# Kernel optimization log

Measured on AMD Instinct MI355X. Metric: run time of the kernel, lower is better.

The kernel has to match this reference:

```python
import jax, jax.numpy as jnp
import numpy as np

B, N, M = 2, 2048, 2048
D = 1024          # query_dim == context_dim == inner_dim
H, DH = 16, 64    # heads, dim_head
SCALE = DH ** -0.5


def setup_inputs() -> dict:
    key = jax.random.key(0)
    ks = jax.random.split(key, 7)
    s = 0.02
    return {
        "x": jax.random.normal(ks[0], (B, N, D), jnp.float32),
        "context": jax.random.normal(ks[1], (B, M, D), jnp.float32),
        "Wq": jax.random.normal(ks[2], (D, H * DH), jnp.float32) * s,
        "Wk": jax.random.normal(ks[3], (D, H * DH), jnp.float32) * s,
        "Wv": jax.random.normal(ks[4], (D, H * DH), jnp.float32) * s,
        "Wo": jax.random.normal(ks[5], (H * DH, D), jnp.float32) * s,
        "bo": jax.random.normal(ks[6], (D,), jnp.float32) * s,
    }


def reference(x, context, Wq, Wk, Wv, Wo, bo):
    # Linear projections (bias-free, as in to_q/to_k/to_v)
    q = (x @ Wq).reshape(B, N, H, DH)        # [B,N,H,DH]
    k = (context @ Wk).reshape(B, M, H, DH)  # [B,M,H,DH]
    v = (context @ Wv).reshape(B, M, H, DH)
    # QK^T * scale, softmax over keys, then AV
    sim = jnp.einsum('bnhd,bmhd->bhnm', q, k) * SCALE  # [B,H,N,M]
    attn = jax.nn.softmax(sim, axis=-1)
    out = jnp.einsum('bhnm,bmhd->bnhd', attn, v)       # [B,N,H,DH]
    out = out.reshape(B, N, H * DH)
    return out @ Wo + bo  # to_out Linear; dropout=0 is identity
```

## Files before the change

### kernel.cpp

```cpp
#include <hip/hip_runtime.h>

#define B_  2
#define N_  2048
#define M_  2048
#define D_  1024
#define H_  16
#define DH_ 64

typedef __bf16 bf16x8 __attribute__((ext_vector_type(8)));
typedef __bf16 bf16x4 __attribute__((ext_vector_type(4)));
typedef short  short4v __attribute__((ext_vector_type(4)));
typedef float  f32x4  __attribute__((ext_vector_type(4)));
typedef unsigned int u32x4v __attribute__((ext_vector_type(4)));

#define GAS(p) ((__attribute__((address_space(1))) void*)(p))
#define LAS(p) ((__attribute__((address_space(3))) void*)(p))

#define QPRESCALE 0.18033688011112042f

__device__ __forceinline__ unsigned short f2bf(float f) {
    unsigned int u = __builtin_bit_cast(unsigned int, f);
    u += 0x7fffu + ((u >> 16) & 1u);
    return (unsigned short)(u >> 16);
}

__device__ __forceinline__ unsigned cvtpkbf(float a, float b) {
    unsigned r;
    asm("v_cvt_pk_bf16_f32 %0, %1, %2" : "=v"(r) : "v"(a), "v"(b));
    return r;
}

__global__ __launch_bounds__(256) void prep(
    const float* __restrict__ x, const float* __restrict__ ctx,
    const float* __restrict__ Wq, const float* __restrict__ Wk,
    const float* __restrict__ Wv, const float* __restrict__ Wo,
    unsigned short* __restrict__ xb, unsigned short* __restrict__ cb,
    unsigned short* __restrict__ WTbase)
{
    if (blockIdx.z == 4) {
        int blk = blockIdx.y * 32 + blockIdx.x;
        int stride = 1024 * 256;
        for (int i = blk * 256 + threadIdx.x; i < 2097152; i += stride) {
            const float4* src; unsigned short* dst; int j;
            if (i < 1048576) { src = (const float4*)x;   dst = xb; j = i; }
            else             { src = (const float4*)ctx; dst = cb; j = i - 1048576; }
            float4 v = src[j];
            ushort4 o = make_ushort4(f2bf(v.x), f2bf(v.y), f2bf(v.z), f2bf(v.w));
            *(ushort4*)(dst + 4*j) = o;
        }
        return;
    }
    const float* W = (blockIdx.z == 0) ? Wq : (blockIdx.z == 1) ? Wk
                    : (blockIdx.z == 2) ? Wv : Wo;
    unsigned short* WT = WTbase + (size_t)blockIdx.z * 1048576;
    __shared__ unsigned short t[32][33];
    int tx = threadIdx.x & 31, ty8 = threadIdx.x >> 5;
    int c = blockIdx.x * 32 + tx;
#pragma unroll
    for (int i = 0; i < 4; ++i) {
        int r = blockIdx.y * 32 + i*8 + ty8;
        t[i*8 + ty8][tx] = f2bf(W[(size_t)r * 1024 + c]);
    }
    __syncthreads();
    int c2 = blockIdx.y * 32 + tx;
#pragma unroll
    for (int i = 0; i < 4; ++i) {
        int r2 = blockIdx.x * 32 + i*8 + ty8;
        WT[(size_t)r2 * 1024 + c2] = t[tx][i*8 + ty8];
    }
}

__global__ __launch_bounds__(256) void gemm128(
    const unsigned short* __restrict__ xb,
    const unsigned short* __restrict__ cb,
    const unsigned short* __restrict__ wT,
    const unsigned short* __restrict__ aoA,
    unsigned short* __restrict__ qkv_out,
    const float* __restrict__ bo,
    float* __restrict__ outF,
    int base_mode)
{
    __shared__ __align__(16) unsigned short As[2][128*32];
    __shared__ __align__(16) unsigned short Bs[2][128*32];

    const int mode = base_mode + blockIdx.z;
    const unsigned short* Amat;
    const unsigned short* Bt;
    if (mode == 0)      { Amat = wT;               Bt = xb; }
    else if (mode == 1) { Amat = wT + 1048576;     Bt = cb; }
    else if (mode == 2) { Amat = cb;               Bt = wT + 2*1048576; }
    else                { Amat = wT + 3*1048576;   Bt = aoA; }

    const int tid = threadIdx.x;
    const int w = tid >> 6, l = tid & 63;
    const int quad = l >> 4, l16 = l & 15;
    const int wm = w & 1, wn = w >> 1;
    int row0, col0;
    if (mode == 2) { row0 = blockIdx.x * 128; col0 = blockIdx.y * 128; }
    else           { row0 = blockIdx.y * 128; col0 = blockIdx.x * 128; }

    f32x4 acc[4][4];
#pragma unroll
    for (int i = 0; i < 4; ++i)
#pragma unroll
        for (int j = 0; j < 4; ++j) acc[i][j] = (f32x4){0.f, 0.f, 0.f, 0.f};

    for (int k0 = 0; k0 < 1024; k0 += 64) {
        __syncthreads();
#pragma unroll
        for (int h = 0; h < 2; ++h) {
#pragma unroll
            for (int i = 0; i < 2; ++i) {
                int s = i*256 + w*64 + l;
                int m = s >> 2, c = s & 3;
                int cs = c ^ ((m >> 1) & 3);
                __builtin_amdgcn_global_load_lds(
                    GAS(Amat + (size_t)(row0 + m)*1024 + k0 + h*32 + cs*8),
                    LAS(As[h] + (i*256 + w*64)*8), 16, 0, 0);
                __builtin_amdgcn_global_load_lds(
                    GAS(Bt + (size_t)(col0 + m)*1024 + k0 + h*32 + cs*8),
                    LAS(Bs[h] + (i*256 + w*64)*8), 16, 0, 0);
            }
        }
        __syncthreads();

#pragma unroll
        for (int h = 0; h < 2; ++h) {
            bf16x8 af[4], bfr[4];
#pragma unroll
            for (int mt = 0; mt < 4; ++mt) {
                int m = wm*64 + mt*16 + l16;
                af[mt] = *reinterpret_cast<const bf16x8*>(As[h] + m*32 + (quad ^ ((m >> 1) & 3))*8);
                int n = wn*64 + mt*16 + l16;
                bfr[mt] = *reinterpret_cast<const bf16x8*>(Bs[h] + n*32 + (quad ^ ((n >> 1) & 3))*8);
            }
#pragma unroll
            for (int mt = 0; mt < 4; ++mt)
#pragma unroll
                for (int nt = 0; nt < 4; ++nt)
                    acc[mt][nt] = __builtin_amdgcn_mfma_f32_16x16x32_bf16(
                        af[mt], bfr[nt], acc[mt][nt], 0, 0, 0);
        }
    }

    if (mode == 2) {
#pragma unroll
        for (int mt = 0; mt < 4; ++mt) {
            int gr = row0 + wm*64 + mt*16 + quad*4;
            int b = gr >> 11, nidx = gr & 2047;
#pragma unroll
            for (int nt = 0; nt < 4; ++nt) {
                int col = col0 + wn*64 + nt*16 + l16;
                int h = col >> 6, d = col & 63;
                ushort4 pk = make_ushort4(f2bf(acc[mt][nt][0]), f2bf(acc[mt][nt][1]),
                                          f2bf(acc[mt][nt][2]), f2bf(acc[mt][nt][3]));
                *(ushort4*)(qkv_out + (size_t)2*4194304
                            + (size_t)((b*16 + h)*64 + d)*2048 + nidx) = pk;
            }
        }
    } else {
        const float qs = (mode == 0) ? QPRESCALE : 1.0f;
        unsigned short* obase = qkv_out + (size_t)mode*4194304;
#pragma unroll
        for (int nt = 0; nt < 4; ++nt) {
            int n = col0 + wn*64 + nt*16 + l16;
            int b = n >> 11, nidx = n & 2047;
#pragma unroll
            for (int mt = 0; mt < 4; ++mt) {
                int c = row0 + wm*64 + mt*16 + quad*4;
                int h = c >> 6, d = c & 63;
                ushort4 pkv = make_ushort4(
                    f2bf(acc[mt][nt][0] * qs), f2bf(acc[mt][nt][1] * qs),
                    f2bf(acc[mt][nt][2] * qs), f2bf(acc[mt][nt][3] * qs));
                *(ushort4*)(obase + (size_t)((b*16 + h)*2048 + nidx)*64 + d) = pkv;
            }
        }
    }
}

__global__ __launch_bounds__(256) void gemm_out(
    const unsigned short* __restrict__ woT,
    const unsigned short* __restrict__ aoA,
    const float* __restrict__ bo,
    float* __restrict__ outF)
{
    __shared__ __align__(16) unsigned short As[64*32];
    __shared__ __align__(16) unsigned short Bs[128*32];

    const int tid = threadIdx.x;
    const int w = tid >> 6, l = tid & 63;
    const int quad = l >> 4, l16 = l & 15;
    const int row0 = blockIdx.y * 64;
    const int col0 = blockIdx.x * 128;

    f32x4 acc[4][2];
#pragma unroll
    for (int i = 0; i < 4; ++i)
#pragma unroll
        for (int j = 0; j < 2; ++j) acc[i][j] = (f32x4){0.f, 0.f, 0.f, 0.f};

    for (int k0 = 0; k0 < 1024; k0 += 32) {
        __syncthreads();
        {
            int m = tid >> 2, c = tid & 3;
            int cs = c ^ ((m >> 1) & 3);
            __builtin_amdgcn_global_load_lds(
                GAS(woT + (size_t)(row0 + m)*1024 + k0 + cs*8),
                LAS(As + (w*64)*8), 16, 0, 0);
        }
#pragma unroll
        for (int i = 0; i < 2; ++i) {
            int s = i*256 + tid;
            int m = s >> 2, c = s & 3;
            int cs = c ^ ((m >> 1) & 3);
            __builtin_amdgcn_global_load_lds(
                GAS(aoA + (size_t)(col0 + m)*1024 + k0 + cs*8),
                LAS(Bs + (i*256 + w*64)*8), 16, 0, 0);
        }
        __syncthreads();

        bf16x8 af[4], bfr[2];
#pragma unroll
        for (int mt = 0; mt < 4; ++mt) {
            int m = mt*16 + l16;
            af[mt] = *reinterpret_cast<const bf16x8*>(As + m*32 + (quad ^ ((m >> 1) & 3))*8);
        }
#pragma unroll
        for (int nt = 0; nt < 2; ++nt) {
            int n = w*32 + nt*16 + l16;
            bfr[nt] = *reinterpret_cast<const bf16x8*>(Bs + n*32 + (quad ^ ((n >> 1) & 3))*8);
        }
#pragma unroll
        for (int mt = 0; mt < 4; ++mt)
#pragma unroll
            for (int nt = 0; nt < 2; ++nt)
                acc[mt][nt] = __builtin_amdgcn_mfma_f32_16x16x32_bf16(
                    af[mt], bfr[nt], acc[mt][nt], 0, 0, 0);
    }

#pragma unroll
    for (int mt = 0; mt < 4; ++mt) {
        int c = row0 + mt*16 + quad*4;
        float4 bv = *(const float4*)(bo + c);
#pragma unroll
        for (int nt = 0; nt < 2; ++nt) {
            int n = col0 + w*32 + nt*16 + l16;
            float4 ov = make_float4(acc[mt][nt][0] + bv.x, acc[mt][nt][1] + bv.y,
                                    acc[mt][nt][2] + bv.z, acc[mt][nt][3] + bv.w);
            *(float4*)(outF + (size_t)n*1024 + c) = ov;
        }
    }
}

__global__ __launch_bounds__(256, 2) void flash_attn(
    const unsigned short* __restrict__ qw,
    const unsigned short* __restrict__ kw,
    const unsigned short* __restrict__ vtw,
    unsigned short* __restrict__ ao)
{
    __shared__ __align__(16) unsigned short Tile[2][9216];

    const int tid = threadIdx.x;
    const int w = tid >> 6, l = tid & 63;
    const int quad = l >> 4, l16 = l & 15;
    const int bh = blockIdx.z * H_ + blockIdx.y;
    const int q0 = blockIdx.x * 128 + w * 32;

    int goff[5];
#pragma unroll
    for (int i = 0; i < 5; ++i) {
        int n = i*256 + w*64 + l;
        int m = (n < 576) ? n : n - 576;
        int row = m / 9, c = m % 9;  if (c > 7) c = 7;
        goff[i] = (n < 576) ? row*64 + c*8 : row*2048 + c*8;
    }
    const unsigned short* kbase = kw + (size_t)bh*131072;
    const unsigned short* vbase = vtw + (size_t)bh*131072;

    bf16x8 qf[2][2];
#pragma unroll
    for (int qg = 0; qg < 2; ++qg)
#pragma unroll
        for (int s = 0; s < 2; ++s)
            qf[qg][s] = *reinterpret_cast<const bf16x8*>(
                qw + (size_t)(bh*2048 + q0 + qg*16 + l16)*64 + s*32 + quad*8);

    f32x4 accO[2][4];
#pragma unroll
    for (int qg = 0; qg < 2; ++qg)
#pragma unroll
        for (int td = 0; td < 4; ++td) accO[qg][td] = (f32x4){0.f, 0.f, 0.f, 0.f};
    float lpart[2] = {0.f, 0.f};

    const f32x4 zz = (f32x4){0.f, 0.f, 0.f, 0.f};

    {
#pragma unroll
        for (int i = 0; i < 4; ++i) {
            const unsigned short* bp = (i*4 + w < 9) ? kbase : vbase;
            __builtin_amdgcn_global_load_lds(GAS(bp + goff[i]),
                LAS(&Tile[0][(i*256 + w*64)*8]), 16, 0, 0);
        }
        if (w < 2)
            __builtin_amdgcn_global_load_lds(GAS(vbase + goff[4]),
                LAS(&Tile[0][(1024 + w*64)*8]), 16, 0, 0);
    }

    for (int it = 0; it < 32; ++it) {
        __syncthreads();
        const int cur = it & 1;

        if (it + 1 < 32) {
            const unsigned short* kp = kbase + (it+1)*4096;
            const unsigned short* vp = vbase + (it+1)*64;
#pragma unroll
            for (int i = 0; i < 4; ++i) {
                const unsigned short* bp = (i*4 + w < 9) ? kp : vp;
                __builtin_amdgcn_global_load_lds(GAS(bp + goff[i]),
                    LAS(&Tile[cur^1][(i*256 + w*64)*8]), 16, 0, 0);
            }
            if (w < 2)
                __builtin_amdgcn_global_load_lds(GAS(vp + goff[4]),
                    LAS(&Tile[cur^1][(1024 + w*64)*8]), 16, 0, 0);
        }

        const unsigned short* Ks = &Tile[cur][0];
        const unsigned short* Vs = &Tile[cur][4608];

        f32x4 sac[2][4];
        __builtin_amdgcn_s_setprio(1);
#pragma unroll
        for (int t = 0; t < 4; ++t) {
            const unsigned short* krow = Ks + (t*16 + l16)*72 + quad*8;
            bf16x8 kf0 = *reinterpret_cast<const bf16x8*>(krow);
            bf16x8 kf1 = *reinterpret_cast<const bf16x8*>(krow + 32);
            sac[0][t] = __builtin_amdgcn_mfma_f32_16x16x32_bf16(kf0, qf[0][0], zz, 0, 0, 0);
            sac[1][t] = __builtin_amdgcn_mfma_f32_16x16x32_bf16(kf0, qf[1][0], zz, 0, 0, 0);
            sac[0][t] = __builtin_amdgcn_mfma_f32_16x16x32_bf16(kf1, qf[0][1], sac[0][t], 0, 0, 0);
            sac[1][t] = __builtin_amdgcn_mfma_f32_16x16x32_bf16(kf1, qf[1][1], sac[1][t], 0, 0, 0);
        }
        __builtin_amdgcn_s_setprio(0);

        u32x4v pB[2][2];
#pragma unroll
        for (int qg = 0; qg < 2; ++qg) {
            float s0 = 0.f, s1 = 0.f, s2 = 0.f, s3 = 0.f;
#pragma unroll
            for (int t2 = 0; t2 < 2; ++t2) {
                float pe0 = __builtin_amdgcn_exp2f(sac[qg][2*t2][0]);
                float pe1 = __builtin_amdgcn_exp2f(sac[qg][2*t2][1]);
                float pe2 = __builtin_amdgcn_exp2f(sac[qg][2*t2][2]);
                float pe3 = __builtin_amdgcn_exp2f(sac[qg][2*t2][3]);
                float po0 = __builtin_amdgcn_exp2f(sac[qg][2*t2+1][0]);
                float po1 = __builtin_amdgcn_exp2f(sac[qg][2*t2+1][1]);
                float po2 = __builtin_amdgcn_exp2f(sac[qg][2*t2+1][2]);
                float po3 = __builtin_amdgcn_exp2f(sac[qg][2*t2+1][3]);
                s0 += pe0 + po0; s1 += pe1 + po1;
                s2 += pe2 + po2; s3 += pe3 + po3;
                unsigned b0 = cvtpkbf(pe0, pe1), b1 = cvtpkbf(pe2, pe3);
                unsigned b2 = cvtpkbf(po0, po1), b3 = cvtpkbf(po2, po3);
                asm("v_permlane32_swap_b32 %0, %1" : "+v"(b0), "+v"(b2));
                asm("v_permlane16_swap_b32 %0, %1" : "+v"(b0), "+v"(b2));
                asm("v_permlane32_swap_b32 %0, %1" : "+v"(b1), "+v"(b3));
                asm("v_permlane16_swap_b32 %0, %1" : "+v"(b1), "+v"(b3));
                pB[qg][t2] = (u32x4v){b0, b1, b2, b3};
            }
            lpart[qg] += (s0 + s1) + (s2 + s3);
        }

        __builtin_amdgcn_s_setprio(1);
#pragma unroll
        for (int td = 0; td < 4; ++td) {
            const unsigned short* vrow = Vs + (td*16 + l16)*72 + quad*8;
#pragma unroll
            for (int t2 = 0; t2 < 2; ++t2) {
                bf16x8 vf = *reinterpret_cast<const bf16x8*>(vrow + t2*32);
                accO[0][td] = __builtin_amdgcn_mfma_f32_16x16x32_bf16(
                    vf, __builtin_bit_cast(bf16x8, pB[0][t2]), accO[0][td], 0, 0, 0);
                accO[1][td] = __builtin_amdgcn_mfma_f32_16x16x32_bf16(
                    vf, __builtin_bit_cast(bf16x8, pB[1][t2]), accO[1][td], 0, 0, 0);
            }
        }
        __builtin_amdgcn_s_setprio(0);
    }

#pragma unroll
    for (int qg = 0; qg < 2; ++qg) {
        float s = lpart[qg];
        s += __shfl_xor(s, 16);
        s += __shfl_xor(s, 32);
        float inv = 1.f / s;
        const size_t rowbase =
            (size_t)(blockIdx.z*2048 + q0 + qg*16 + l16)*1024 + blockIdx.y*64;
#pragma unroll
        for (int td = 0; td < 4; ++td)
#pragma unroll
            for (int r = 0; r < 4; ++r)
                ao[rowbase + td*16 + quad*4 + r] = f2bf(accO[qg][td][r] * inv);
    }
}

extern "C" void kernel_launch(void* const* d_in, const int* in_sizes, int n_in,
                              void* d_out, int out_size, void* d_ws, size_t ws_size,
                              hipStream_t stream)
{
    const float* x   = (const float*)d_in[0];
    const float* ctx = (const float*)d_in[1];
    const float* Wq  = (const float*)d_in[2];
    const float* Wk  = (const float*)d_in[3];
    const float* Wv  = (const float*)d_in[4];
    const float* Wo  = (const float*)d_in[5];
    const float* bo  = (const float*)d_in[6];
    float* out = (float*)d_out;

    unsigned short* ws  = (unsigned short*)d_ws;
    unsigned short* xb  = ws;
    unsigned short* cb  = ws + 4194304;
    unsigned short* wT  = ws + 8388608;
    unsigned short* qkv = ws + 12582912;
    unsigned short* ao  = ws;

    prep<<<dim3(32, 32, 5), dim3(256), 0, stream>>>(x, ctx, Wq, Wk, Wv, Wo, xb, cb, wT);
    gemm128<<<dim3(32, 8, 3), dim3(256), 0, stream>>>(xb, cb, wT, ao, qkv, bo, out, 0);
    flash_attn<<<dim3(16, 16, 2), dim3(256), 0, stream>>>(qkv, qkv + 4194304, qkv + 8388608, ao);
    gemm_out<<<dim3(32, 16), dim3(256), 0, stream>>>(wT + 3*1048576, ao, bo, out);
}
```

Measured before the change: 201.0 us.

## Split KV tile across warp pairs in flash attention; double K-step in out-proj GEMM

Flash attention now gives each warp 64 queries and half of each 64-key tile, instead of 32 queries over all keys. This halves the K/V LDS fragment reads per query and lets each loaded K/V fragment feed four MFMAs. The two halves' partial outputs and row sums are reduced through LDS at the end. The output-projection GEMM now loads two 32-wide K slices per barrier pair, halving the number of syncs. The cost is more registers per warp in attention, an extra LDS reduction step, and only half the warps doing the final store.

```diff
diff --git a/kernel.cpp b/kernel.cpp
--- a/kernel.cpp
+++ b/kernel.cpp
@@ -184,8 +184,8 @@
     const float* __restrict__ bo,
     float* __restrict__ outF)
 {
-    __shared__ __align__(16) unsigned short As[64*32];
-    __shared__ __align__(16) unsigned short Bs[128*32];
+    __shared__ __align__(16) unsigned short As[2][64*32];
+    __shared__ __align__(16) unsigned short Bs[2][128*32];
 
     const int tid = threadIdx.x;
     const int w = tid >> 6, l = tid & 63;
@@ -199,43 +199,49 @@
 #pragma unroll
         for (int j = 0; j < 2; ++j) acc[i][j] = (f32x4){0.f, 0.f, 0.f, 0.f};
 
-    for (int k0 = 0; k0 < 1024; k0 += 32) {
+    for (int k0 = 0; k0 < 1024; k0 += 64) {
         __syncthreads();
-        {
-            int m = tid >> 2, c = tid & 3;
-            int cs = c ^ ((m >> 1) & 3);
-            __builtin_amdgcn_global_load_lds(
-                GAS(woT + (size_t)(row0 + m)*1024 + k0 + cs*8),
-                LAS(As + (w*64)*8), 16, 0, 0);
-        }
-#pragma unroll
-        for (int i = 0; i < 2; ++i) {
-            int s = i*256 + tid;
-            int m = s >> 2, c = s & 3;
-            int cs = c ^ ((m >> 1) & 3);
-            __builtin_amdgcn_global_load_lds(
-                GAS(aoA + (size_t)(col0 + m)*1024 + k0 + cs*8),
-                LAS(Bs + (i*256 + w*64)*8), 16, 0, 0);
+#pragma unroll
+        for (int h = 0; h < 2; ++h) {
+            {
+                int m = tid >> 2, c = tid & 3;
+                int cs = c ^ ((m >> 1) & 3);
+                __builtin_amdgcn_global_load_lds(
+                    GAS(woT + (size_t)(row0 + m)*1024 + k0 + h*32 + cs*8),
+                    LAS(As[h] + (w*64)*8), 16, 0, 0);
+            }
+#pragma unroll
+            for (int i = 0; i < 2; ++i) {
+                int s = i*256 + tid;
+                int m = s >> 2, c = s & 3;
+                int cs = c ^ ((m >> 1) & 3);
+                __builtin_amdgcn_global_load_lds(
+                    GAS(aoA + (size_t)(col0 + m)*1024 + k0 + h*32 + cs*8),
+                    LAS(Bs[h] + (i*256 + w*64)*8), 16, 0, 0);
+            }
         }
         __syncthreads();
 
-        bf16x8 af[4], bfr[2];
-#pragma unroll
-        for (int mt = 0; mt < 4; ++mt) {
-            int m = mt*16 + l16;
-            af[mt] = *reinterpret_cast<const bf16x8*>(As + m*32 + (quad ^ ((m >> 1) & 3))*8);
-        }
-#pragma unroll
-        for (int nt = 0; nt < 2; ++nt) {
-            int n = w*32 + nt*16 + l16;
-            bfr[nt] = *reinterpret_cast<const bf16x8*>(Bs + n*32 + (quad ^ ((n >> 1) & 3))*8);
-        }
-#pragma unroll
-        for (int mt = 0; mt < 4; ++mt)
-#pragma unroll
-            for (int nt = 0; nt < 2; ++nt)
-                acc[mt][nt] = __builtin_amdgcn_mfma_f32_16x16x32_bf16(
-                    af[mt], bfr[nt], acc[mt][nt], 0, 0, 0);
+#pragma unroll
+        for (int h = 0; h < 2; ++h) {
+            bf16x8 af[4], bfr[2];
+#pragma unroll
+            for (int mt = 0; mt < 4; ++mt) {
+                int m = mt*16 + l16;
+                af[mt] = *reinterpret_cast<const bf16x8*>(As[h] + m*32 + (quad ^ ((m >> 1) & 3))*8);
+            }
+#pragma unroll
+            for (int nt = 0; nt < 2; ++nt) {
+                int n = w*32 + nt*16 + l16;
+                bfr[nt] = *reinterpret_cast<const bf16x8*>(Bs[h] + n*32 + (quad ^ ((n >> 1) & 3))*8);
+            }
+#pragma unroll
+            for (int mt = 0; mt < 4; ++mt)
+#pragma unroll
+                for (int nt = 0; nt < 2; ++nt)
+                    acc[mt][nt] = __builtin_amdgcn_mfma_f32_16x16x32_bf16(
+                        af[mt], bfr[nt], acc[mt][nt], 0, 0, 0);
+        }
     }
 
 #pragma unroll
@@ -264,7 +270,8 @@
     const int w = tid >> 6, l = tid & 63;
     const int quad = l >> 4, l16 = l & 15;
     const int bh = blockIdx.z * H_ + blockIdx.y;
-    const int q0 = blockIdx.x * 128 + w * 32;
+    const int qh = w & 1, kvh = w >> 1;
+    const int q0 = blockIdx.x * 128 + qh * 64;
 
     int goff[5];
 #pragma unroll
@@ -277,20 +284,20 @@
     const unsigned short* kbase = kw + (size_t)bh*131072;
     const unsigned short* vbase = vtw + (size_t)bh*131072;
 
-    bf16x8 qf[2][2];
-#pragma unroll
-    for (int qg = 0; qg < 2; ++qg)
+    bf16x8 qf[4][2];
+#pragma unroll
+    for (int qg = 0; qg < 4; ++qg)
 #pragma unroll
         for (int s = 0; s < 2; ++s)
             qf[qg][s] = *reinterpret_cast<const bf16x8*>(
                 qw + (size_t)(bh*2048 + q0 + qg*16 + l16)*64 + s*32 + quad*8);
 
-    f32x4 accO[2][4];
-#pragma unroll
-    for (int qg = 0; qg < 2; ++qg)
+    f32x4 accO[4][4];
+#pragma unroll
+    for (int qg = 0; qg < 4; ++qg)
 #pragma unroll
         for (int td = 0; td < 4; ++td) accO[qg][td] = (f32x4){0.f, 0.f, 0.f, 0.f};
-    float lpart[2] = {0.f, 0.f};
+    float lpart[4] = {0.f, 0.f, 0.f, 0.f};
 
     const f32x4 zz = (f32x4){0.f, 0.f, 0.f, 0.f};
 
@@ -327,76 +334,92 @@
         const unsigned short* Ks = &Tile[cur][0];
         const unsigned short* Vs = &Tile[cur][4608];
 
-        f32x4 sac[2][4];
+        f32x4 sac[4][2];
         __builtin_amdgcn_s_setprio(1);
 #pragma unroll
-        for (int t = 0; t < 4; ++t) {
-            const unsigned short* krow = Ks + (t*16 + l16)*72 + quad*8;
+        for (int t = 0; t < 2; ++t) {
+            const unsigned short* krow = Ks + (kvh*32 + t*16 + l16)*72 + quad*8;
             bf16x8 kf0 = *reinterpret_cast<const bf16x8*>(krow);
             bf16x8 kf1 = *reinterpret_cast<const bf16x8*>(krow + 32);
-            sac[0][t] = __builtin_amdgcn_mfma_f32_16x16x32_bf16(kf0, qf[0][0], zz, 0, 0, 0);
-            sac[1][t] = __builtin_amdgcn_mfma_f32_16x16x32_bf16(kf0, qf[1][0], zz, 0, 0, 0);
-            sac[0][t] = __builtin_amdgcn_mfma_f32_16x16x32_bf16(kf1, qf[0][1], sac[0][t], 0, 0, 0);
-            sac[1][t] = __builtin_amdgcn_mfma_f32_16x16x32_bf16(kf1, qf[1][1], sac[1][t], 0, 0, 0);
+#pragma unroll
+            for (int qg = 0; qg < 4; ++qg) {
+                sac[qg][t] = __builtin_amdgcn_mfma_f32_16x16x32_bf16(kf0, qf[qg][0], zz, 0, 0, 0);
+                sac[qg][t] = __builtin_amdgcn_mfma_f32_16x16x32_bf16(kf1, qf[qg][1], sac[qg][t], 0, 0, 0);
+            }
         }
         __builtin_amdgcn_s_setprio(0);
 
-        u32x4v pB[2][2];
-#pragma unroll
-        for (int qg = 0; qg < 2; ++qg) {
-            float s0 = 0.f, s1 = 0.f, s2 = 0.f, s3 = 0.f;
-#pragma unroll
-            for (int t2 = 0; t2 < 2; ++t2) {
-                float pe0 = __builtin_amdgcn_exp2f(sac[qg][2*t2][0]);
-                float pe1 = __builtin_amdgcn_exp2f(sac[qg][2*t2][1]);
-                float pe2 = __builtin_amdgcn_exp2f(sac[qg][2*t2][2]);
-                float pe3 = __builtin_amdgcn_exp2f(sac[qg][2*t2][3]);
-                float po0 = __builtin_amdgcn_exp2f(sac[qg][2*t2+1][0]);
-                float po1 = __builtin_amdgcn_exp2f(sac[qg][2*t2+1][1]);
-                float po2 = __builtin_amdgcn_exp2f(sac[qg][2*t2+1][2]);
-                float po3 = __builtin_amdgcn_exp2f(sac[qg][2*t2+1][3]);
-                s0 += pe0 + po0; s1 += pe1 + po1;
-                s2 += pe2 + po2; s3 += pe3 + po3;
-                unsigned b0 = cvtpkbf(pe0, pe1), b1 = cvtpkbf(pe2, pe3);
-                unsigned b2 = cvtpkbf(po0, po1), b3 = cvtpkbf(po2, po3);
-                asm("v_permlane32_swap_b32 %0, %1" : "+v"(b0), "+v"(b2));
-                asm("v_permlane16_swap_b32 %0, %1" : "+v"(b0), "+v"(b2));
-                asm("v_permlane32_swap_b32 %0, %1" : "+v"(b1), "+v"(b3));
-                asm("v_permlane16_swap_b32 %0, %1" : "+v"(b1), "+v"(b3));
-                pB[qg][t2] = (u32x4v){b0, b1, b2, b3};
-            }
-            lpart[qg] += (s0 + s1) + (s2 + s3);
+        u32x4v pB[4];
+#pragma unroll
+        for (int qg = 0; qg < 4; ++qg) {
+            float pe0 = __builtin_amdgcn_exp2f(sac[qg][0][0]);
+            float pe1 = __builtin_amdgcn_exp2f(sac[qg][0][1]);
+            float pe2 = __builtin_amdgcn_exp2f(sac[qg][0][2]);
+            float pe3 = __builtin_amdgcn_exp2f(sac[qg][0][3]);
+            float po0 = __builtin_amdgcn_exp2f(sac[qg][1][0]);
+            float po1 = __builtin_amdgcn_exp2f(sac[qg][1][1]);
+            float po2 = __builtin_amdgcn_exp2f(sac[qg][1][2]);
+            float po3 = __builtin_amdgcn_exp2f(sac[qg][1][3]);
+            lpart[qg] += ((pe0 + po0) + (pe1 + po1)) + ((pe2 + po2) + (pe3 + po3));
+            unsigned b0 = cvtpkbf(pe0, pe1), b1 = cvtpkbf(pe2, pe3);
+            unsigned b2 = cvtpkbf(po0, po1), b3 = cvtpkbf(po2, po3);
+            asm("v_permlane32_swap_b32 %0, %1" : "+v"(b0), "+v"(b2));
+            asm("v_permlane16_swap_b32 %0, %1" : "+v"(b0), "+v"(b2));
+            asm("v_permlane32_swap_b32 %0, %1" : "+v"(b1), "+v"(b3));
+            asm("v_permlane16_swap_b32 %0, %1" : "+v"(b1), "+v"(b3));
+            pB[qg] = (u32x4v){b0, b1, b2, b3};
         }
 
         __builtin_amdgcn_s_setprio(1);
 #pragma unroll
         for (int td = 0; td < 4; ++td) {
-            const unsigned short* vrow = Vs + (td*16 + l16)*72 + quad*8;
-#pragma unroll
-            for (int t2 = 0; t2 < 2; ++t2) {
-                bf16x8 vf = *reinterpret_cast<const bf16x8*>(vrow + t2*32);
-                accO[0][td] = __builtin_amdgcn_mfma_f32_16x16x32_bf16(
-                    vf, __builtin_bit_cast(bf16x8, pB[0][t2]), accO[0][td], 0, 0, 0);
-                accO[1][td] = __builtin_amdgcn_mfma_f32_16x16x32_bf16(
-                    vf, __builtin_bit_cast(bf16x8, pB[1][t2]), accO[1][td], 0, 0, 0);
-            }
+            bf16x8 vf = *reinterpret_cast<const bf16x8*>(
+                Vs + (td*16 + l16)*72 + kvh*32 + quad*8);
+#pragma unroll
+            for (int qg = 0; qg < 4; ++qg)
+                accO[qg][td] = __builtin_amdgcn_mfma_f32_16x16x32_bf16(
+                    vf, __builtin_bit_cast(bf16x8, pB[qg]), accO[qg][td], 0, 0, 0);
         }
         __builtin_amdgcn_s_setprio(0);
     }
 
-#pragma unroll
-    for (int qg = 0; qg < 2; ++qg) {
-        float s = lpart[qg];
-        s += __shfl_xor(s, 16);
-        s += __shfl_xor(s, 32);
-        float inv = 1.f / s;
-        const size_t rowbase =
-            (size_t)(blockIdx.z*2048 + q0 + qg*16 + l16)*1024 + blockIdx.y*64;
-#pragma unroll
-        for (int td = 0; td < 4; ++td)
-#pragma unroll
-            for (int r = 0; r < 4; ++r)
-                ao[rowbase + td*16 + quad*4 + r] = f2bf(accO[qg][td][r] * inv);
+    float* xch = (float*)&Tile[0][0];
+    __syncthreads();
+    if (kvh == 1) {
+        float* base = xch + (size_t)(qh*64 + l)*72;
+#pragma unroll
+        for (int qg = 0; qg < 4; ++qg)
+#pragma unroll
+            for (int td = 0; td < 4; ++td)
+                *(f32x4*)(base + (qg*4 + td)*4) = accO[qg][td];
+        *(f32x4*)(base + 64) = (f32x4){lpart[0], lpart[1], lpart[2], lpart[3]};
+    }
+    __syncthreads();
+    if (kvh == 0) {
+        const float* base = xch + (size_t)(qh*64 + l)*72;
+#pragma unroll
+        for (int qg = 0; qg < 4; ++qg)
+#pragma unroll
+            for (int td = 0; td < 4; ++td)
+                accO[qg][td] += *(const f32x4*)(base + (qg*4 + td)*4);
+        f32x4 lp2 = *(const f32x4*)(base + 64);
+        lpart[0] += lp2[0]; lpart[1] += lp2[1];
+        lpart[2] += lp2[2]; lpart[3] += lp2[3];
+
+#pragma unroll
+        for (int qg = 0; qg < 4; ++qg) {
+            float s = lpart[qg];
+            s += __shfl_xor(s, 16);
+            s += __shfl_xor(s, 32);
+            float inv = 1.f / s;
+            const size_t rowbase =
+                (size_t)(blockIdx.z*2048 + q0 + qg*16 + l16)*1024 + blockIdx.y*64;
+#pragma unroll
+            for (int td = 0; td < 4; ++td)
+#pragma unroll
+                for (int r = 0; r < 4; ++r)
+                    ao[rowbase + td*16 + quad*4 + r] = f2bf(accO[qg][td][r] * inv);
+        }
     }
 }
 
```

After: 198.6 us. Within noise of the previous version (-1.2%).
